# Kernel optimization log

Hardware: AMD Instinct MI355X
Metric: run time of the kernel (lower is better)

The kernel has to match this reference:

```python
import jax, jax.numpy as jnp
import numpy as np
import math

MUL = 128
N_NODES = 10000
N_EDGES = 131072
AVG_NEIGH = 16.0
# (l1 of node irrep, l2 of edge SH, output l3); sorted by output irrep like e3nn Irreps.sort
INSTR = [(0, 0, 0), (1, 1, 0), (0, 1, 1), (1, 0, 1), (1, 2, 1), (0, 2, 2), (1, 1, 2), (1, 3, 2), (0, 3, 3), (1, 2, 3)]
SH_OFF = [0, 1, 4, 9]  # offsets of l-blocks inside edge_attrs (dim 16 = 1+3+5+7)


def _su2_cg(j1, j2, j3):
    f = math.factorial
    C = np.zeros((2 * j1 + 1, 2 * j2 + 1, 2 * j3 + 1))
    for m1 in range(-j1, j1 + 1):
        for m2 in range(-j2, j2 + 1):
            m3 = m1 + m2
            if abs(m3) > j3:
                continue
            pref = (2 * j3 + 1) * f(j3 + j1 - j2) * f(j3 - j1 + j2) * f(j1 + j2 - j3) / f(j1 + j2 + j3 + 1)
            pref *= f(j3 + m3) * f(j3 - m3) * f(j1 - m1) * f(j1 + m1) * f(j2 - m2) * f(j2 + m2)
            s = 0.0
            for k in range(max(0, -(j3 - j2 + m1), -(j3 - j1 - m2)), min(j1 + j2 - j3, j1 - m1, j2 + m2) + 1):
                s += (-1.0) ** k / (f(k) * f(j1 + j2 - j3 - k) * f(j1 - m1 - k) * f(j2 + m2 - k) * f(j3 - j2 + m1 + k) * f(j3 - j1 - m2 + k))
            C[m1 + j1, m2 + j2, m3 + j3] = math.sqrt(pref) * s
    return C


def _q(l):
    # change of basis real->complex spherical harmonics (e3nn convention incl. (-i)^l phase)
    q = np.zeros((2 * l + 1, 2 * l + 1), dtype=np.complex128)
    for m in range(-l, 0):
        q[l + m, l + abs(m)] = 1 / math.sqrt(2)
        q[l + m, l - abs(m)] = -1j / math.sqrt(2)
    q[l, l] = 1.0
    for m in range(1, l + 1):
        q[l + m, l + abs(m)] = (-1) ** m / math.sqrt(2)
        q[l + m, l - abs(m)] = 1j * (-1) ** m / math.sqrt(2)
    return ((-1j) ** l) * q


def _w3j(l1, l2, l3):
    C = _su2_cg(l1, l2, l3).astype(np.complex128)
    Q1, Q2, Q3 = _q(l1), _q(l2), _q(l3)
    for q3 in (np.conj(Q3), Q3):
        D = np.einsum('abc,ai,bj,ck->ijk', C, Q1, Q2, q3)
        if np.abs(D.imag).max() < 1e-9:
            Dr = D.real
            return (Dr / np.linalg.norm(Dr)).astype(np.float32)
    raise ValueError('real wigner-3j construction failed')


W3J = {ins: _w3j(ins[0], ins[1], ins[2]) for ins in set(INSTR)}


def setup_inputs():
    ks = jax.random.split(jax.random.key(0), 15)
    return {
        'node_feats': jax.random.normal(ks[0], (N_NODES, 4 * MUL), jnp.float32),
        'node_attrs': jax.random.normal(ks[1], (N_NODES, 10), jnp.float32),
        'edge_attrs': jax.random.normal(ks[2], (N_EDGES, 16), jnp.float32),
        'edge_feats': jax.random.normal(ks[3], (N_EDGES, 8), jnp.float32),
        'edge_index': jax.random.randint(ks[4], (2, N_EDGES), 0, N_NODES, jnp.int32),
        'W_node_0': jax.random.normal(ks[5], (MUL, MUL), jnp.float32),
        'W_node_1': jax.random.normal(ks[6], (MUL, MUL), jnp.float32),
        'R_W0': jax.random.normal(ks[7], (8, 64), jnp.float32),
        'R_W1': jax.random.normal(ks[8], (64, 64), jnp.float32),
        'R_W2': jax.random.normal(ks[9], (64, 64), jnp.float32),
        'R_W3': jax.random.normal(ks[10], (64, len(INSTR) * MUL), jnp.float32),
        'W_out_0': jax.random.normal(ks[11], (2 * MUL, MUL), jnp.float32),
        'W_out_1': jax.random.normal(ks[12], (3 * MUL, MUL), jnp.float32),
        'W_out_2': jax.random.normal(ks[13], (3 * MUL, MUL), jnp.float32),
        'W_out_3': jax.random.normal(ks[14], (2 * MUL, MUL), jnp.float32),
    }


def reference(node_feats, node_attrs, edge_attrs, edge_feats, edge_index, W_node_0, W_node_1, R_W0, R_W1, R_W2, R_W3, W_out_0, W_out_1, W_out_2, W_out_3):
    sender, receiver = edge_index[0], edge_index[1]
    n = node_feats.shape[0]
    # self-interaction Linear (e3nn: per-irrep matmul, weight / sqrt(fan_in))
    h0 = jnp.einsum('nui,uv->nvi', node_feats[:, :MUL].reshape(n, MUL, 1), W_node_0) / math.sqrt(MUL)
    h1 = jnp.einsum('nui,uv->nvi', node_feats[:, MUL:].reshape(n, MUL, 3), W_node_1) / math.sqrt(MUL)
    # radial MLP [8,64,64,64,1280] with SiLU on hidden layers
    r = edge_feats
    for W in (R_W0, R_W1, R_W2):
        r = jax.nn.silu(r @ (W / math.sqrt(W.shape[0])))
    r = r @ (R_W3 / math.sqrt(R_W3.shape[0]))
    hs = (h0[sender], h1[sender])  # gather sender feats, [E, MUL, 2l1+1]
    outs = {0: [], 1: [], 2: [], 3: []}
    for k, (l1, l2, l3) in enumerate(INSTR):
        w3j = jnp.asarray(W3J[(l1, l2, l3)])
        sh = edge_attrs[:, SH_OFF[l2]:SH_OFF[l2] + 2 * l2 + 1]
        w = r[:, k * MUL:(k + 1) * MUL]
        hw = hs[l1] * w[:, :, None]                                    # radial-weighted sender feats
        c = jnp.einsum('ijk,ej->eik', w3j, sh)                         # [E, 2l1+1, 2l3+1]
        t = jnp.einsum('eik,eui->euk', c, hw) * math.sqrt(2 * l3 + 1)  # 'uvu' path, component-norm path weight
        outs[l3].append(jax.ops.segment_sum(t, receiver, num_segments=n))
    Wout = (W_out_0, W_out_1, W_out_2, W_out_3)
    blocks = []
    for l in range(4):
        cat = jnp.concatenate(outs[l], axis=1)  # simplify(): concat multiplicities per l
        blocks.append(jnp.einsum('nui,uv->nvi', cat, Wout[l]) / (math.sqrt(cat.shape[1]) * AVG_NEIGH))
    return jnp.concatenate(blocks, axis=-1)  # reshape_irreps -> [N, MUL, 16]
```

## Files before the change

### kernel.cpp

```cpp
#include <hip/hip_runtime.h>
#include <math.h>

#define NNODES 10000
#define NEDGES 131072
#define CHUNK 16

#define W3J_OFF 0
#define H_OFF   1280
#define R2_OFF  (1280 + NNODES*512)
#define CSR_W   (R2_OFF + NEDGES*64)
#define CNT_W   CSR_W
#define CUR_W   (CSR_W + NNODES)
#define OFF_W   (CSR_W + 2*NNODES)
#define ELIST_W (CSR_W + 2*NNODES + NNODES + 1)

constexpr int cL1[10]  = {0,1,0,1,1,0,1,1,0,1};
constexpr int cL2[10]  = {0,1,1,0,2,2,1,3,3,2};
constexpr int cN3[10]  = {1,1,3,3,3,5,5,5,7,7};
constexpr int cSHO[10] = {0,1,1,0,4,4,1,9,9,4};
constexpr int cCCO[11] = {0,1,4,7,16,25,30,45,60,67,88};
constexpr int cCATO[10]= {0,128,256,640,1024,1408,2048,2688,3328,4224};

struct cpx { double re, im; };
__device__ inline cpx cmul(cpx a, cpx b){ return {a.re*b.re - a.im*b.im, a.re*b.im + a.im*b.re}; }

__device__ double dfact(int n){ double r = 1.0; for (int i = 2; i <= n; ++i) r *= (double)i; return r; }

__device__ double cgval(int j1,int j2,int j3,int m1,int m2){
  int m3 = m1 + m2;
  if (m3 > j3 || m3 < -j3) return 0.0;
  double pref = (double)(2*j3+1) * dfact(j3+j1-j2)*dfact(j3-j1+j2)*dfact(j1+j2-j3)/dfact(j1+j2+j3+1);
  pref *= dfact(j3+m3)*dfact(j3-m3)*dfact(j1-m1)*dfact(j1+m1)*dfact(j2-m2)*dfact(j2+m2);
  int k0 = 0; if (-(j3-j2+m1) > k0) k0 = -(j3-j2+m1); if (-(j3-j1-m2) > k0) k0 = -(j3-j1-m2);
  int k1 = j1+j2-j3; if (j1-m1 < k1) k1 = j1-m1; if (j2+m2 < k1) k1 = j2+m2;
  double s = 0.0;
  for (int k = k0; k <= k1; ++k){
    double d = dfact(k)*dfact(j1+j2-j3-k)*dfact(j1-m1-k)*dfact(j2+m2-k)*dfact(j3-j2+m1+k)*dfact(j3-j1-m2+k);
    s += ((k & 1) ? -1.0 : 1.0) / d;
  }
  return sqrt(pref) * s;
}

__device__ cpx qval(int l, int a, int col){
  int m = a - l;
  const double is2 = 0.70710678118654752440;
  double re = 0.0, im = 0.0;
  if (m < 0){
    if (col == l - m) re = is2;
    else if (col == l + m) im = -is2;
  } else if (m == 0){
    if (col == l) re = 1.0;
  } else {
    double sgn = (m & 1) ? -1.0 : 1.0;
    if (col == l + m) re = sgn * is2;
    else if (col == l - m) im = sgn * is2;
  }
  double pr, pi;
  switch (l & 3){ case 0: pr=1; pi=0; break; case 1: pr=0; pi=-1; break; case 2: pr=-1; pi=0; break; default: pr=0; pi=1; }
  return { re*pr - im*pi, re*pi + im*pr };
}

__global__ void w3j_kernel(float* ws){
  __shared__ double red[128];
  __shared__ int useConjS;
  __shared__ double normS;
  const int IL[10][3] = {{0,0,0},{1,1,0},{0,1,1},{1,0,1},{1,2,1},{0,2,2},{1,1,2},{1,3,2},{0,3,3},{1,2,3}};
  int k = blockIdx.x;
  int l1 = IL[k][0], l2 = IL[k][1], l3 = IL[k][2];
  int n1 = 2*l1+1, n2 = 2*l2+1, n3 = 2*l3+1;
  int nent = n1*n2*n3;
  int tid = threadIdx.x;
  double dcr=0, dci=0, dpr=0, dpi=0;
  if (tid < nent){
    int i = tid/(n2*n3), j = (tid/n3)%n2, kk = tid%n3;
    for (int a = 0; a < n1; ++a){
      for (int b = 0; b < n2; ++b){
        int m1 = a - l1, m2 = b - l2, m3 = m1 + m2;
        if (m3 < -l3 || m3 > l3) continue;
        int c = m3 + l3;
        double C = cgval(l1,l2,l3,m1,m2);
        if (C == 0.0) continue;
        cpx q1 = qval(l1,a,i), q2 = qval(l2,b,j), q3 = qval(l3,c,kk);
        cpx t = cmul(q1,q2);
        cpx q3c = { q3.re, -q3.im };
        cpx tc = cmul(t, q3c);
        cpx tp = cmul(t, q3);
        dcr += C*tc.re; dci += C*tc.im;
        dpr += C*tp.re; dpi += C*tp.im;
      }
    }
  }
  red[tid] = (tid < nent) ? fabs(dci) : 0.0;
  __syncthreads();
  if (tid == 0){
    double mx = 0.0;
    for (int t = 0; t < 128; ++t) if (red[t] > mx) mx = red[t];
    useConjS = (mx < 1e-9) ? 1 : 0;
  }
  __syncthreads();
  double re = useConjS ? dcr : dpr;
  red[tid] = (tid < nent) ? re*re : 0.0;
  __syncthreads();
  if (tid == 0){
    double s = 0.0;
    for (int t = 0; t < 128; ++t) s += red[t];
    normS = sqrt(s);
  }
  __syncthreads();
  if (tid < nent)
    ws[W3J_OFF + k*128 + tid] = (float)(re / normS * sqrt((double)(2*l3+1)));
}

__launch_bounds__(256, 4)
__global__ void node_kernel(const float* __restrict__ nf, const float* __restrict__ W0,
                            const float* __restrict__ W1, float* __restrict__ ws){
  __shared__ float AtL[128*68];
  float* h = ws + H_OFF;
  int tid = threadIdx.x;
  int n0 = blockIdx.x * 64;
  const float rs = 0.08838834764831845f;
  int mg = (tid & 15) * 4;
  int vg = (tid >> 4) * 8;
  for (int c = 0; c < 4; ++c){
    __syncthreads();
    for (int idx = tid; idx < 8192; idx += 256){
      int m = idx >> 7, u = idx & 127;
      int node = n0 + m;
      float v = 0.f;
      if (node < NNODES)
        v = (c == 0) ? nf[(size_t)node*512 + u] : nf[(size_t)node*512 + 128 + u*3 + (c-1)];
      AtL[u*68 + m] = v;
    }
    __syncthreads();
    const float* W = (c == 0) ? W0 : W1;
    float acc[8][4];
    #pragma unroll
    for (int a = 0; a < 8; ++a){ acc[a][0]=0.f; acc[a][1]=0.f; acc[a][2]=0.f; acc[a][3]=0.f; }
    for (int u = 0; u < 128; ++u){
      float4 am = *(const float4*)&AtL[u*68 + mg];
      const float* wr = W + u*128 + vg;
      float4 b0 = *(const float4*)wr;
      float4 b1 = *(const float4*)(wr + 4);
      float aa[4] = {am.x, am.y, am.z, am.w};
      float bb[8] = {b0.x,b0.y,b0.z,b0.w,b1.x,b1.y,b1.z,b1.w};
      #pragma unroll
      for (int a = 0; a < 8; ++a)
        #pragma unroll
        for (int e = 0; e < 4; ++e)
          acc[a][e] += bb[a]*aa[e];
    }
    #pragma unroll
    for (int e = 0; e < 4; ++e){
      int node = n0 + mg + e;
      if (node < NNODES){
        float4 s0 = {acc[0][e]*rs, acc[1][e]*rs, acc[2][e]*rs, acc[3][e]*rs};
        float4 s1 = {acc[4][e]*rs, acc[5][e]*rs, acc[6][e]*rs, acc[7][e]*rs};
        *(float4*)&h[(size_t)node*512 + c*128 + vg] = s0;
        *(float4*)&h[(size_t)node*512 + c*128 + vg + 4] = s1;
      }
    }
  }
}

template<int KDIM>
__device__ __forceinline__ void mlp_layer(const float* __restrict__ Wg, const float* aL,
                                          float* oL, int tid, float scale){
  int eg = (tid & 15) * 4;
  int jg = (tid >> 4) * 4;
  float acc[4][4];
  #pragma unroll
  for (int a = 0; a < 4; ++a){ acc[a][0]=0.f; acc[a][1]=0.f; acc[a][2]=0.f; acc[a][3]=0.f; }
  #pragma unroll 4
  for (int i = 0; i < KDIM; ++i){
    float4 a4 = *(const float4*)&aL[i*68 + eg];
    float4 b4 = *(const float4*)&Wg[i*64 + jg];
    float aa[4] = {a4.x,a4.y,a4.z,a4.w};
    float bb[4] = {b4.x,b4.y,b4.z,b4.w};
    #pragma unroll
    for (int a = 0; a < 4; ++a)
      #pragma unroll
      for (int e = 0; e < 4; ++e)
        acc[a][e] += bb[a]*aa[e];
  }
  #pragma unroll
  for (int a = 0; a < 4; ++a){
    float4 st;
    float x0 = acc[a][0]*scale; st.x = x0/(1.f + expf(-x0));
    float x1 = acc[a][1]*scale; st.y = x1/(1.f + expf(-x1));
    float x2 = acc[a][2]*scale; st.z = x2/(1.f + expf(-x2));
    float x3 = acc[a][3]*scale; st.w = x3/(1.f + expf(-x3));
    *(float4*)&oL[(jg+a)*68 + eg] = st;
  }
}

__launch_bounds__(256)
__global__ void r2_kernel(const float* __restrict__ ef,
                          const float* __restrict__ RW0, const float* __restrict__ RW1,
                          const float* __restrict__ RW2, float* __restrict__ wsf){
  __shared__ float bufA[64*68];
  __shared__ float bufB[64*68];
  __shared__ float r2T[64*68];
  float* R2 = wsf + R2_OFF;
  int tid = threadIdx.x;
  int eb = blockIdx.x * 64;
  float* efT = r2T;
  for (int idx = tid; idx < 512; idx += 256){
    int e = idx >> 3, i2 = idx & 7;
    efT[i2*68 + e] = ef[(size_t)(eb+e)*8 + i2];
  }
  __syncthreads();
  mlp_layer<8 >(RW0, efT, bufA, tid, 0.35355339059327373f);
  __syncthreads();
  mlp_layer<64>(RW1, bufA, bufB, tid, 0.125f);
  __syncthreads();
  mlp_layer<64>(RW2, bufB, r2T, tid, 0.125f);
  __syncthreads();
  for (int idx = tid; idx < 4096; idx += 256){
    int e = idx >> 6, i = idx & 63;
    R2[((size_t)(eb+e) << 6) + i] = r2T[i*68 + e];
  }
}

__global__ void hist_kernel(const int* __restrict__ ei, int* __restrict__ cnt){
  int e = blockIdx.x*256 + threadIdx.x;
  if (e < NEDGES) atomicAdd(&cnt[ei[NEDGES + e]], 1);
}

__global__ void scan_kernel(const int* __restrict__ cnt, int* __restrict__ off){
  __shared__ int part[256];
  __shared__ int partp[256];
  int t = threadIdx.x;
  const int S = 40;
  int s = 0;
  for (int j = 0; j < S; ++j){ int idx = t*S + j; if (idx < NNODES) s += cnt[idx]; }
  part[t] = s;
  __syncthreads();
  if (t == 0){ int run = 0; for (int i = 0; i < 256; ++i){ partp[i] = run; run += part[i]; } }
  __syncthreads();
  int run = partp[t];
  for (int j = 0; j < S; ++j){
    int idx = t*S + j;
    if (idx <= NNODES){
      off[idx] = run;
      if (idx < NNODES) run += cnt[idx];
    }
  }
}

__global__ void fill_kernel(const int* __restrict__ ei, const int* __restrict__ off,
                            int* __restrict__ cur, int* __restrict__ elist){
  int e = blockIdx.x*256 + threadIdx.x;
  if (e < NEDGES){
    int r = ei[NEDGES + e];
    int p = off[r] + atomicAdd(&cur[r], 1);
    elist[p] = e;
  }
}

__device__ __forceinline__ float cc_compute(int r, const float* w3L, const float* she){
  float v = 0.f;
  #pragma unroll
  for (int in = 0; in < 10; ++in){
    if (r >= cCCO[in] && r < cCCO[in+1]){
      int rr = r - cCCO[in];
      const int N3v = cN3[in];
      const int N2v = 2*cL2[in] + 1;
      int i = rr / N3v;
      int q = rr - i*N3v;
      float s = 0.f;
      for (int j = 0; j < N2v; ++j)
        s += w3L[in*128 + (i*N2v + j)*N3v + q] * she[cSHO[in] + j];
      v = s;
    }
  }
  return v;
}

template<int IN>
__device__ __forceinline__ void tp_g(const float* __restrict__ cce, const float* __restrict__ hp,
                                     float wv, float* accm){
  constexpr int N3v = cN3[IN];
  if constexpr (cL1[IN] == 0){
    float wh = wv * hp[0];
    #pragma unroll
    for (int q = 0; q < N3v; ++q) accm[q] += cce[q] * wh;
  } else {
    float wa = wv * hp[128];
    float wb = wv * hp[256];
    float wc = wv * hp[384];
    #pragma unroll
    for (int q = 0; q < N3v; ++q)
      accm[q] += cce[q]*wa + cce[N3v+q]*wb + cce[2*N3v+q]*wc;
  }
}

template<int M>
__device__ __forceinline__ void do_m(const float* __restrict__ RW3, const float* r2L,
                                     const float* ccL, const float* __restrict__ h,
                                     const int* sC, int tid, int u, int i0, float* accm){
  float wv[CHUNK];
  #pragma unroll
  for (int e = 0; e < CHUNK; ++e) wv[e] = 0.f;
  const float* rw = RW3 + 256*M + tid;
  #pragma unroll 4
  for (int i = 0; i < 64; ++i){
    float b = rw[(size_t)i*1280];
    const float* rr = &r2L[i*20];
    float4 r0 = *(const float4*)&rr[0];
    float4 r1 = *(const float4*)&rr[4];
    float4 r2v= *(const float4*)&rr[8];
    float4 r3 = *(const float4*)&rr[12];
    wv[0]  += b*r0.x;  wv[1]  += b*r0.y;  wv[2]  += b*r0.z;  wv[3]  += b*r0.w;
    wv[4]  += b*r1.x;  wv[5]  += b*r1.y;  wv[6]  += b*r1.z;  wv[7]  += b*r1.w;
    wv[8]  += b*r2v.x; wv[9]  += b*r2v.y; wv[10] += b*r2v.z; wv[11] += b*r2v.w;
    wv[12] += b*r3.x;  wv[13] += b*r3.y;  wv[14] += b*r3.z;  wv[15] += b*r3.w;
  }
  #pragma unroll
  for (int e = 0; e < CHUNK; ++e) wv[e] *= 0.125f;
  #pragma unroll
  for (int eh = 0; eh < 2; ++eh){
    if (i0 == 0){
      #pragma unroll
      for (int e8 = 0; e8 < 8; ++e8){
        int e = eh*8 + e8;
        const float* hp = h + ((size_t)sC[e] << 9) + u;
        tp_g<2*M>(ccL + e*88 + cCCO[2*M], hp, wv[e], accm);
      }
    } else {
      #pragma unroll
      for (int e8 = 0; e8 < 8; ++e8){
        int e = eh*8 + e8;
        const float* hp = h + ((size_t)sC[e] << 9) + u;
        tp_g<2*M+1>(ccL + e*88 + cCCO[2*M+1], hp, wv[e], accm);
      }
    }
  }
}

template<int IN>
__device__ __forceinline__ void st_cat(float* catL, int u, const float* accm){
  constexpr int N3v = cN3[IN];
  float* p = catL + cCATO[IN] + u*N3v;
  #pragma unroll
  for (int q = 0; q < N3v; ++q) p[q] = accm[q];
}

template<int L>
__device__ __forceinline__ void out_g(const float* catL, const float* __restrict__ Wo,
                                      float* redL, float* __restrict__ outp,
                                      int n, int v, int half){
  constexpr int NI = 2*L + 1;
  constexpr int UL = (L==0 || L==3) ? 256 : 384;
  constexpr int GOv = (L==0) ? 0 : (L==1) ? 256 : (L==2) ? 1408 : 3328;
  constexpr int OOv = (L==0) ? 0 : (L==1) ? 1 : (L==2) ? 4 : 9;
  const float scale = (L==0 || L==3) ? 0.00390625f : 0.0031894435433133252f;
  float o[NI];
  #pragma unroll
  for (int i = 0; i < NI; ++i) o[i] = 0.f;
  int ul0 = half * (UL/2);
  for (int ul = ul0; ul < ul0 + UL/2; ++ul){
    float wv = Wo[(size_t)ul*128 + v];
    const float* a = catL + GOv + ul*NI;
    #pragma unroll
    for (int i = 0; i < NI; ++i) o[i] += a[i]*wv;
  }
  if (half == 1){
    #pragma unroll
    for (int i = 0; i < NI; ++i) redL[v*NI + i] = o[i];
  }
  __syncthreads();
  if (half == 0){
    float* op = outp + (size_t)n*2048 + v*16 + OOv;
    #pragma unroll
    for (int i = 0; i < NI; ++i) op[i] = (o[i] + redL[v*NI + i]) * scale;
  }
  __syncthreads();
}

__launch_bounds__(256, 4)
__global__ void gather_kernel(const float* __restrict__ ea, const int* __restrict__ ei,
                              const float* __restrict__ RW3,
                              const float* __restrict__ Wo0, const float* __restrict__ Wo1,
                              const float* __restrict__ Wo2, const float* __restrict__ Wo3,
                              const float* __restrict__ wsf,
                              const int* __restrict__ off, const int* __restrict__ elist,
                              float* __restrict__ outp){
  __shared__ float smemF[6016];
  int*   idsL = (int*)smemF;
  int*   idsC = (int*)(smemF + 512);
  int*   sC   = (int*)(smemF + 528);
  float* w3L  = smemF + 544;
  float* r2L  = smemF + 1824;
  float* shL  = smemF + 3104;
  float* ccL  = smemF + 3360;
  float* catL = smemF;
  float* redL = smemF + 5120;

  const float* h  = wsf + H_OFF;
  const float* R2 = wsf + R2_OFF;
  int nblk = blockIdx.x, tid = threadIdx.x;
  for (int idx = tid; idx < 1280; idx += 256) w3L[idx] = wsf[W3J_OFF + idx];
  int beg = off[nblk], end = off[nblk+1];
  int deg = end - beg;
  int degc = deg < 512 ? deg : 512;
  for (int idx = tid; idx < degc; idx += 256) idsL[idx] = elist[beg + idx];
  __syncthreads();
  {
    int v0 = 0, r0 = 0, v1 = 0, r1 = 0;
    bool a0 = tid < degc, a1 = tid + 256 < degc;
    if (a0){ v0 = idsL[tid]; int r = 0; for (int j = 0; j < degc; ++j) r += (idsL[j] < v0); r0 = r; }
    if (a1){ v1 = idsL[tid+256]; int r = 0; for (int j = 0; j < degc; ++j) r += (idsL[j] < v1); r1 = r; }
    __syncthreads();
    if (a0) idsL[r0] = v0;
    if (a1) idsL[r1] = v1;
  }

  int u = tid & 127;
  int i0 = tid >> 7;
  float acc0[1] = {0.f};
  float acc1[3] = {0.f,0.f,0.f};
  float acc2[5] = {0.f,0.f,0.f,0.f,0.f};
  float acc3[5] = {0.f,0.f,0.f,0.f,0.f};
  float acc4[7] = {0.f,0.f,0.f,0.f,0.f,0.f,0.f};

  for (int base = 0; base < deg; base += CHUNK){
    int eN = deg - base; if (eN > CHUNK) eN = CHUNK;
    __syncthreads();
    if (tid < CHUNK){
      int k = base + tid;
      int id;
      if (tid < eN) id = (k < degc) ? idsL[k] : elist[beg + k];
      else          id = (base < degc) ? idsL[base] : elist[beg + base];
      idsC[tid] = id;
      sC[tid]   = ei[id];
    }
    __syncthreads();
    for (int idx = tid; idx < (CHUNK << 6); idx += 256){
      int e = idx >> 6, i = idx & 63;
      r2L[i*20 + e] = (e < eN) ? R2[((size_t)idsC[e] << 6) + i] : 0.f;
    }
    for (int idx = tid; idx < (CHUNK << 4); idx += 256){
      int e = idx >> 4, j = idx & 15;
      shL[e*16 + j] = ea[((size_t)idsC[e] << 4) + j];
    }
    __syncthreads();
    for (int idx = tid; idx < CHUNK*88; idx += 256){
      int e = idx / 88, r = idx - e*88;
      ccL[e*88 + r] = cc_compute(r, w3L, shL + e*16);
    }
    __syncthreads();
    do_m<0>(RW3, r2L, ccL, h, sC, tid, u, i0, acc0);
    do_m<1>(RW3, r2L, ccL, h, sC, tid, u, i0, acc1);
    do_m<2>(RW3, r2L, ccL, h, sC, tid, u, i0, acc2);
    do_m<3>(RW3, r2L, ccL, h, sC, tid, u, i0, acc3);
    do_m<4>(RW3, r2L, ccL, h, sC, tid, u, i0, acc4);
  }
  __syncthreads();
  if (i0 == 0){
    st_cat<0>(catL, u, acc0);
    st_cat<2>(catL, u, acc1);
    st_cat<4>(catL, u, acc2);
    st_cat<6>(catL, u, acc3);
    st_cat<8>(catL, u, acc4);
  } else {
    st_cat<1>(catL, u, acc0);
    st_cat<3>(catL, u, acc1);
    st_cat<5>(catL, u, acc2);
    st_cat<7>(catL, u, acc3);
    st_cat<9>(catL, u, acc4);
  }
  __syncthreads();
  out_g<0>(catL, Wo0, redL, outp, nblk, u, i0);
  out_g<1>(catL, Wo1, redL, outp, nblk, u, i0);
  out_g<2>(catL, Wo2, redL, outp, nblk, u, i0);
  out_g<3>(catL, Wo3, redL, outp, nblk, u, i0);
}

extern "C" void kernel_launch(void* const* d_in, const int* in_sizes, int n_in,
                              void* d_out, int out_size, void* d_ws, size_t ws_size,
                              hipStream_t stream){
  const float* nf  = (const float*)d_in[0];
  const float* ea  = (const float*)d_in[2];
  const float* ef  = (const float*)d_in[3];
  const int*   ei  = (const int*)d_in[4];
  const float* W0  = (const float*)d_in[5];
  const float* W1  = (const float*)d_in[6];
  const float* RW0 = (const float*)d_in[7];
  const float* RW1 = (const float*)d_in[8];
  const float* RW2 = (const float*)d_in[9];
  const float* RW3 = (const float*)d_in[10];
  const float* Wo0 = (const float*)d_in[11];
  const float* Wo1 = (const float*)d_in[12];
  const float* Wo2 = (const float*)d_in[13];
  const float* Wo3 = (const float*)d_in[14];
  float* wsf  = (float*)d_ws;
  int*   wsi  = (int*)d_ws;
  float* outp = (float*)d_out;

  hipMemsetAsync(wsi + CNT_W, 0, 2*NNODES*sizeof(int), stream);
  w3j_kernel<<<10, 128, 0, stream>>>(wsf);
  node_kernel<<<157, 256, 0, stream>>>(nf, W0, W1, wsf);
  r2_kernel<<<2048, 256, 0, stream>>>(ef, RW0, RW1, RW2, wsf);
  hist_kernel<<<512, 256, 0, stream>>>(ei, wsi + CNT_W);
  scan_kernel<<<1, 256, 0, stream>>>(wsi + CNT_W, wsi + OFF_W);
  fill_kernel<<<512, 256, 0, stream>>>(ei, wsi + OFF_W, wsi + CUR_W, wsi + ELIST_W);
  gather_kernel<<<NNODES, 256, 0, stream>>>(ea, ei, RW3, Wo0, Wo1, Wo2, Wo3,
                                            wsf, wsi + OFF_W, wsi + ELIST_W, outp);
}
```

Before: 1.893 ms.

## Precompute per-edge coupling coefficients in separate kernel; split output projection by l

Adds a cc_kernel that computes the 88 per-edge Wigner-3j × spherical-harmonic coefficients once into workspace, so the gather kernel just loads them instead of recomputing from shared w3j and SH. This removes the w3j and SH shared buffers and one barrier per chunk. The output projection now has each half-block handle two whole l-blocks, with no shared reduction and fewer barriers. Shared memory shrinks and launch bounds rise to 7 blocks per CU. The cost is an extra kernel plus roughly 46 MB of extra workspace traffic.

```diff
diff --git a/kernel.cpp b/kernel.cpp
--- a/kernel.cpp
+++ b/kernel.cpp
@@ -8,7 +8,8 @@
 #define W3J_OFF 0
 #define H_OFF   1280
 #define R2_OFF  (1280 + NNODES*512)
-#define CSR_W   (R2_OFF + NEDGES*64)
+#define CC_OFF  (R2_OFF + NEDGES*64)
+#define CSR_W   (CC_OFF + NEDGES*88)
 #define CNT_W   CSR_W
 #define CUR_W   (CSR_W + NNODES)
 #define OFF_W   (CSR_W + 2*NNODES)
@@ -221,42 +222,6 @@
   }
 }
 
-__global__ void hist_kernel(const int* __restrict__ ei, int* __restrict__ cnt){
-  int e = blockIdx.x*256 + threadIdx.x;
-  if (e < NEDGES) atomicAdd(&cnt[ei[NEDGES + e]], 1);
-}
-
-__global__ void scan_kernel(const int* __restrict__ cnt, int* __restrict__ off){
-  __shared__ int part[256];
-  __shared__ int partp[256];
-  int t = threadIdx.x;
-  const int S = 40;
-  int s = 0;
-  for (int j = 0; j < S; ++j){ int idx = t*S + j; if (idx < NNODES) s += cnt[idx]; }
-  part[t] = s;
-  __syncthreads();
-  if (t == 0){ int run = 0; for (int i = 0; i < 256; ++i){ partp[i] = run; run += part[i]; } }
-  __syncthreads();
-  int run = partp[t];
-  for (int j = 0; j < S; ++j){
-    int idx = t*S + j;
-    if (idx <= NNODES){
-      off[idx] = run;
-      if (idx < NNODES) run += cnt[idx];
-    }
-  }
-}
-
-__global__ void fill_kernel(const int* __restrict__ ei, const int* __restrict__ off,
-                            int* __restrict__ cur, int* __restrict__ elist){
-  int e = blockIdx.x*256 + threadIdx.x;
-  if (e < NEDGES){
-    int r = ei[NEDGES + e];
-    int p = off[r] + atomicAdd(&cur[r], 1);
-    elist[p] = e;
-  }
-}
-
 __device__ __forceinline__ float cc_compute(int r, const float* w3L, const float* she){
   float v = 0.f;
   #pragma unroll
@@ -274,6 +239,61 @@
     }
   }
   return v;
+}
+
+__launch_bounds__(256)
+__global__ void cc_kernel(const float* __restrict__ ea, float* __restrict__ wsf){
+  __shared__ float w3L[1280];
+  __shared__ float shE[32*16];
+  float* ccG = wsf + CC_OFF;
+  int tid = threadIdx.x;
+  int eb = blockIdx.x * 32;
+  for (int idx = tid; idx < 1280; idx += 256) w3L[idx] = wsf[W3J_OFF + idx];
+  for (int idx = tid; idx < 512; idx += 256){
+    int e = idx >> 4, j = idx & 15;
+    shE[e*16 + j] = ea[((size_t)(eb+e) << 4) + j];
+  }
+  __syncthreads();
+  for (int idx = tid; idx < 32*88; idx += 256){
+    int e = idx / 88, r = idx - e*88;
+    ccG[(size_t)(eb+e)*88 + r] = cc_compute(r, w3L, shE + e*16);
+  }
+}
+
+__global__ void hist_kernel(const int* __restrict__ ei, int* __restrict__ cnt){
+  int e = blockIdx.x*256 + threadIdx.x;
+  if (e < NEDGES) atomicAdd(&cnt[ei[NEDGES + e]], 1);
+}
+
+__global__ void scan_kernel(const int* __restrict__ cnt, int* __restrict__ off){
+  __shared__ int part[256];
+  __shared__ int partp[256];
+  int t = threadIdx.x;
+  const int S = 40;
+  int s = 0;
+  for (int j = 0; j < S; ++j){ int idx = t*S + j; if (idx < NNODES) s += cnt[idx]; }
+  part[t] = s;
+  __syncthreads();
+  if (t == 0){ int run = 0; for (int i = 0; i < 256; ++i){ partp[i] = run; run += part[i]; } }
+  __syncthreads();
+  int run = partp[t];
+  for (int j = 0; j < S; ++j){
+    int idx = t*S + j;
+    if (idx <= NNODES){
+      off[idx] = run;
+      if (idx < NNODES) run += cnt[idx];
+    }
+  }
+}
+
+__global__ void fill_kernel(const int* __restrict__ ei, const int* __restrict__ off,
+                            int* __restrict__ cur, int* __restrict__ elist){
+  int e = blockIdx.x*256 + threadIdx.x;
+  if (e < NEDGES){
+    int r = ei[NEDGES + e];
+    int p = off[r] + atomicAdd(&cur[r], 1);
+    elist[p] = e;
+  }
 }
 
 template<int IN>
@@ -346,9 +366,8 @@
 }
 
 template<int L>
-__device__ __forceinline__ void out_g(const float* catL, const float* __restrict__ Wo,
-                                      float* redL, float* __restrict__ outp,
-                                      int n, int v, int half){
+__device__ __forceinline__ void out_l(const float* catL, const float* __restrict__ Wo,
+                                      float* __restrict__ outp, int n, int v){
   constexpr int NI = 2*L + 1;
   constexpr int UL = (L==0 || L==3) ? 256 : 384;
   constexpr int GOv = (L==0) ? 0 : (L==1) ? 256 : (L==2) ? 1408 : 3328;
@@ -357,49 +376,38 @@
   float o[NI];
   #pragma unroll
   for (int i = 0; i < NI; ++i) o[i] = 0.f;
-  int ul0 = half * (UL/2);
-  for (int ul = ul0; ul < ul0 + UL/2; ++ul){
+  #pragma unroll 4
+  for (int ul = 0; ul < UL; ++ul){
     float wv = Wo[(size_t)ul*128 + v];
     const float* a = catL + GOv + ul*NI;
     #pragma unroll
     for (int i = 0; i < NI; ++i) o[i] += a[i]*wv;
   }
-  if (half == 1){
-    #pragma unroll
-    for (int i = 0; i < NI; ++i) redL[v*NI + i] = o[i];
-  }
-  __syncthreads();
-  if (half == 0){
-    float* op = outp + (size_t)n*2048 + v*16 + OOv;
-    #pragma unroll
-    for (int i = 0; i < NI; ++i) op[i] = (o[i] + redL[v*NI + i]) * scale;
-  }
-  __syncthreads();
-}
-
-__launch_bounds__(256, 4)
-__global__ void gather_kernel(const float* __restrict__ ea, const int* __restrict__ ei,
+  float* op = outp + (size_t)n*2048 + v*16 + OOv;
+  #pragma unroll
+  for (int i = 0; i < NI; ++i) op[i] = o[i]*scale;
+}
+
+__launch_bounds__(256, 7)
+__global__ void gather_kernel(const int* __restrict__ ei,
                               const float* __restrict__ RW3,
                               const float* __restrict__ Wo0, const float* __restrict__ Wo1,
                               const float* __restrict__ Wo2, const float* __restrict__ Wo3,
                               const float* __restrict__ wsf,
                               const int* __restrict__ off, const int* __restrict__ elist,
                               float* __restrict__ outp){
-  __shared__ float smemF[6016];
+  __shared__ float smemF[5120];
   int*   idsL = (int*)smemF;
   int*   idsC = (int*)(smemF + 512);
   int*   sC   = (int*)(smemF + 528);
-  float* w3L  = smemF + 544;
-  float* r2L  = smemF + 1824;
-  float* shL  = smemF + 3104;
-  float* ccL  = smemF + 3360;
+  float* r2L  = smemF + 544;
+  float* ccL  = smemF + 1824;
   float* catL = smemF;
-  float* redL = smemF + 5120;
-
-  const float* h  = wsf + H_OFF;
-  const float* R2 = wsf + R2_OFF;
+
+  const float* h   = wsf + H_OFF;
+  const float* R2  = wsf + R2_OFF;
+  const float* ccG = wsf + CC_OFF;
   int nblk = blockIdx.x, tid = threadIdx.x;
-  for (int idx = tid; idx < 1280; idx += 256) w3L[idx] = wsf[W3J_OFF + idx];
   int beg = off[nblk], end = off[nblk+1];
   int deg = end - beg;
   int degc = deg < 512 ? deg : 512;
@@ -439,14 +447,9 @@
       int e = idx >> 6, i = idx & 63;
       r2L[i*20 + e] = (e < eN) ? R2[((size_t)idsC[e] << 6) + i] : 0.f;
     }
-    for (int idx = tid; idx < (CHUNK << 4); idx += 256){
-      int e = idx >> 4, j = idx & 15;
-      shL[e*16 + j] = ea[((size_t)idsC[e] << 4) + j];
-    }
-    __syncthreads();
     for (int idx = tid; idx < CHUNK*88; idx += 256){
       int e = idx / 88, r = idx - e*88;
-      ccL[e*88 + r] = cc_compute(r, w3L, shL + e*16);
+      ccL[idx] = ccG[(size_t)idsC[e]*88 + r];
     }
     __syncthreads();
     do_m<0>(RW3, r2L, ccL, h, sC, tid, u, i0, acc0);
@@ -470,10 +473,13 @@
     st_cat<9>(catL, u, acc4);
   }
   __syncthreads();
-  out_g<0>(catL, Wo0, redL, outp, nblk, u, i0);
-  out_g<1>(catL, Wo1, redL, outp, nblk, u, i0);
-  out_g<2>(catL, Wo2, redL, outp, nblk, u, i0);
-  out_g<3>(catL, Wo3, redL, outp, nblk, u, i0);
+  if (i0 == 0){
+    out_l<0>(catL, Wo0, outp, nblk, u);
+    out_l<2>(catL, Wo2, outp, nblk, u);
+  } else {
+    out_l<1>(catL, Wo1, outp, nblk, u);
+    out_l<3>(catL, Wo3, outp, nblk, u);
+  }
 }
 
 extern "C" void kernel_launch(void* const* d_in, const int* in_sizes, int n_in,
@@ -501,9 +507,10 @@
   w3j_kernel<<<10, 128, 0, stream>>>(wsf);
   node_kernel<<<157, 256, 0, stream>>>(nf, W0, W1, wsf);
   r2_kernel<<<2048, 256, 0, stream>>>(ef, RW0, RW1, RW2, wsf);
+  cc_kernel<<<4096, 256, 0, stream>>>(ea, wsf);
   hist_kernel<<<512, 256, 0, stream>>>(ei, wsi + CNT_W);
   scan_kernel<<<1, 256, 0, stream>>>(wsi + CNT_W, wsi + OFF_W);
   fill_kernel<<<512, 256, 0, stream>>>(ei, wsi + OFF_W, wsi + CUR_W, wsi + ELIST_W);
-  gather_kernel<<<NNODES, 256, 0, stream>>>(ea, ei, RW3, Wo0, Wo1, Wo2, Wo3,
+  gather_kernel<<<NNODES, 256, 0, stream>>>(ei, RW3, Wo0, Wo1, Wo2, Wo3,
                                             wsf, wsi + OFF_W, wsi + ELIST_W, outp);
 }
```

Measured after the change: 1.792 ms. 5.3% less time.
